# Optimization experiments

Hardware: AMD Instinct MI355X
Metric: run time of the kernel (lower is better)

Reference implementation:

```python
import jax, jax.numpy as jnp
import numpy as np

Q_AA = 21    # amino acids + gap
D_REP = 64   # representation dim
H = 32       # heads
L = 256      # sequence length
DK = 32
DV = 32
M = 8192     # number of MSA sequences
LAMBDA = 1e-3


def setup_inputs() -> dict:
    key = jax.random.key(0)
    ks = jax.random.split(key, 6)
    return {
        "reps_matrix": jax.random.normal(ks[0], (Q_AA, D_REP), jnp.float32),
        "Q": jax.random.normal(ks[1], (H, L, DK), jnp.float32),
        "K": jax.random.normal(ks[2], (H, L, DK), jnp.float32),
        "V_metric": jax.random.normal(ks[3], (H, D_REP, DV), jnp.float32),
        "Z": jax.random.randint(ks[4], (L, M), 0, Q_AA),
        "weights": jax.random.uniform(ks[5], (M,), jnp.float32),
    }


def reference(reps_matrix, Q, K, V_metric, Z, weights):
    dk = Q.shape[-1]
    # symmetrized per-head attention map (no mask)
    scores = jnp.einsum('hid,hjd->hij', Q, K) / jnp.sqrt(jnp.asarray(dk, Q.dtype))
    probs = jax.nn.softmax(scores, axis=-1)
    A = 0.5 * (probs + jnp.swapaxes(probs, -1, -2))        # (H, L, L)

    # V_aa via RBF kernel on V1 = reps_matrix @ V_metric
    V1 = jnp.einsum('qd,hdv->hqv', reps_matrix, V_metric)  # (H, q, dv)
    gamma = 1.0 / V1.shape[1]  # torch code uses 1/X.shape[1] == 1/q
    sq = jnp.sum(V1 * V1, axis=-1)                          # (H, q)
    D2 = sq[:, :, None] + sq[:, None, :] - 2.0 * jnp.einsum('hqv,hav->hqa', V1, V1)
    Vaa = jnp.exp(-gamma * jnp.maximum(D2, 0.0))           # (H, q, q)

    # coupling tensor J with zeroed diagonal (i == j)
    J = jnp.einsum('hij,hqa->ijqa', A, Vaa)                # (L, L, q, q)
    off_diag = 1.0 - jnp.eye(J.shape[0], dtype=J.dtype)
    J = J * off_diag[:, :, None, None]

    q = Vaa.shape[1]
    Zoh = jax.nn.one_hot(Z, q, dtype=J.dtype)              # (L, M, q)
    # energy[state, position, sequence] = sum_{j,a} J[r,j,state,a] * onehot(Z)[j,m,a]
    E = jnp.einsum('rjqa,jma->qrm', J, Zoh)                # (q, L, M)
    lge = jax.nn.logsumexp(E, axis=0)                      # (L, M)
    E_correct = jnp.take_along_axis(E, Z[None], axis=0)[0] # (L, M)

    pl = -jnp.sum(weights * jnp.sum(E_correct - lge, axis=0))
    reg = LAMBDA * jnp.sum(J * J)
    return pl + reg
```

## Files before the change

### kernel.cpp

```cpp
#include <hip/hip_runtime.h>
#include <hip/hip_bf16.h>

#define H_ 32
#define L_ 256
#define DK_ 32
#define DV_ 32
#define QAA 21
#define AQ_ 441
#define DREP 64
#define M_ 8192
#define LAMBDA_ 1e-3f

#define JSTR 56
#define JJSTR 1184
#define JCH 8
#define CHUNK_B (JCH * JJSTR)
#define NCH (L_ / JCH)

#define JC 8
#define TM 4

__global__ __launch_bounds__(256) void softmax_kernel(const float* __restrict__ Q,
                                                      const float* __restrict__ K,
                                                      float* __restrict__ P) {
  const int i = blockIdx.x, h = blockIdx.y, j = threadIdx.x;
  __shared__ float qrow[DK_];
  __shared__ float red[256];
  if (j < DK_) qrow[j] = Q[(h * L_ + i) * DK_ + j];
  __syncthreads();
  const float* krow = &K[(h * L_ + j) * DK_];
  float s = 0.f;
#pragma unroll
  for (int d = 0; d < DK_; ++d) s += qrow[d] * krow[d];
  s *= 0.17677669529663687f;
  red[j] = s;
  __syncthreads();
  for (int t = 128; t > 0; t >>= 1) {
    if (j < t) red[j] = fmaxf(red[j], red[j + t]);
    __syncthreads();
  }
  const float mx = red[0];
  __syncthreads();
  const float e = __expf(s - mx);
  red[j] = e;
  __syncthreads();
  for (int t = 128; t > 0; t >>= 1) {
    if (j < t) red[j] += red[j + t];
    __syncthreads();
  }
  P[(h * L_ + i) * L_ + j] = e / red[0];
}

__global__ __launch_bounds__(256) void sym_kernel(const float* __restrict__ P,
                                                  float* __restrict__ A) {
  const int idx = blockIdx.x * 256 + threadIdx.x;
  const int h = idx >> 16;
  const int i = (idx >> 8) & 255;
  const int j = idx & 255;
  A[idx] = 0.5f * (P[idx] + P[(h << 16) | (j << 8) | i]);
}

__global__ __launch_bounds__(256) void vaa_kernel(const float* __restrict__ reps,
                                                  const float* __restrict__ Vm,
                                                  float* __restrict__ Vaa) {
  const int h = blockIdx.x;
  __shared__ float V1[QAA * DV_];
  __shared__ float sq[QAA];
  for (int e = threadIdx.x; e < QAA * DV_; e += 256) {
    const int q = e >> 5, v = e & 31;
    float acc = 0.f;
#pragma unroll
    for (int d = 0; d < DREP; ++d) acc += reps[q * DREP + d] * Vm[(h * DREP + d) * DV_ + v];
    V1[e] = acc;
  }
  __syncthreads();
  if (threadIdx.x < QAA) {
    float acc = 0.f;
#pragma unroll
    for (int v = 0; v < DV_; ++v) { const float x = V1[threadIdx.x * DV_ + v]; acc += x * x; }
    sq[threadIdx.x] = acc;
  }
  __syncthreads();
  const float gamma = 1.f / 21.f;
  for (int e = threadIdx.x; e < AQ_; e += 256) {
    const int qq = e / QAA, aa = e - qq * QAA;
    float dot = 0.f;
#pragma unroll
    for (int v = 0; v < DV_; ++v) dot += V1[qq * DV_ + v] * V1[aa * DV_ + v];
    const float d2 = sq[qq] + sq[aa] - 2.f * dot;
    Vaa[h * AQ_ + e] = __expf(-gamma * fmaxf(d2, 0.f));
  }
}

__global__ __launch_bounds__(256) void reg_kernel(const float* __restrict__ A,
                                                  const float* __restrict__ Vaa,
                                                  float* __restrict__ out) {
  const int h1 = blockIdx.x >> 5, h2 = blockIdx.x & 31;
  const float* A1 = A + h1 * (L_ * L_);
  const float* A2 = A + h2 * (L_ * L_);
  float s = 0.f;
  for (int idx = threadIdx.x; idx < L_ * L_; idx += 256) s += A1[idx] * A2[idx];
  s -= A1[threadIdx.x * (L_ + 1)] * A2[threadIdx.x * (L_ + 1)];
  float g = 0.f;
  const float* V1 = Vaa + h1 * AQ_;
  const float* V2 = Vaa + h2 * AQ_;
  for (int e = threadIdx.x; e < AQ_; e += 256) g += V1[e] * V2[e];
  __shared__ float redS[256], redG[256];
  redS[threadIdx.x] = s; redG[threadIdx.x] = g;
  __syncthreads();
  for (int t = 128; t > 0; t >>= 1) {
    if (threadIdx.x < t) {
      redS[threadIdx.x] += redS[threadIdx.x + t];
      redG[threadIdx.x] += redG[threadIdx.x + t];
    }
    __syncthreads();
  }
  if (threadIdx.x == 0) atomicAdd(out, LAMBDA_ * redS[0] * redG[0]);
}

static __device__ inline unsigned bf16_bits(float x) {
  __hip_bfloat16 b = __float2bfloat16(x);
  unsigned short u;
  __builtin_memcpy(&u, &b, 2);
  return (unsigned)u;
}

__global__ __launch_bounds__(256) void jbuild_kernel(const float* __restrict__ A,
                                                     const float* __restrict__ Vaa,
                                                     unsigned char* __restrict__ Jg) {
  __shared__ float AT[L_ * H_];
  const int r = blockIdx.x, tid = threadIdx.x;
#pragma unroll
  for (int i = 0; i < H_; ++i) AT[tid * H_ + i] = A[(i * L_ + r) * L_ + tid];

  const int s = tid;
  const bool active = (s < 252);
  int a = 0, w = 0;
  if (active) { a = s / 12; w = s - a * 12; }
  const int q0 = 2 * w, q1 = q0 + 1;
  float vh0[H_], vh1[H_];
#pragma unroll
  for (int h = 0; h < H_; ++h) {
    vh0[h] = (active && q0 < QAA) ? Vaa[h * AQ_ + a * QAA + q0] : 0.f;
    vh1[h] = (active && q1 < QAA) ? Vaa[h * AQ_ + a * QAA + q1] : 0.f;
  }
  __syncthreads();

  unsigned char* dst = Jg + (size_t)r * (L_ * JJSTR);
  const int byte_off = a * JSTR + w * 4;
  for (int j = 0; j < L_; ++j) {
    float v0 = 0.f, v1 = 0.f;
    const float4* Ar4 = (const float4*)&AT[j * H_];
#pragma unroll
    for (int h4 = 0; h4 < H_ / 4; ++h4) {
      const float4 a4 = Ar4[h4];
      v0 += a4.x * vh0[h4 * 4 + 0]; v1 += a4.x * vh1[h4 * 4 + 0];
      v0 += a4.y * vh0[h4 * 4 + 1]; v1 += a4.y * vh1[h4 * 4 + 1];
      v0 += a4.z * vh0[h4 * 4 + 2]; v1 += a4.z * vh1[h4 * 4 + 2];
      v0 += a4.w * vh0[h4 * 4 + 3]; v1 += a4.w * vh1[h4 * 4 + 3];
    }
    if (j == r) { v0 = 0.f; v1 = 0.f; }
    if (active) {
      const unsigned u = bf16_bits(v0) | (bf16_bits(v1) << 16);
      *(unsigned*)(dst + (size_t)(j * JJSTR + byte_off)) = u;
    }
  }
}

__global__ __launch_bounds__(256) void gather_kernel(const unsigned char* __restrict__ Jg,
                                                     const int* __restrict__ Z,
                                                     const float* __restrict__ W,
                                                     float* __restrict__ out) {
  __shared__ __align__(16) unsigned char buf[CHUNK_B];
  __shared__ float red[256];
  const int r = blockIdx.x, tid = threadIdx.x;
  const int mb = blockIdx.y * 1024 + tid * 4;
  const unsigned char* Jr = Jg + (size_t)r * (L_ * JJSTR);

  float E[TM][QAA];
#pragma unroll
  for (int k = 0; k < TM; ++k)
#pragma unroll
    for (int q = 0; q < QAA; ++q) E[k][q] = 0.f;

  uint4 st0, st1, st2;
  const int i0 = tid, i1 = 256 + tid, i2 = 512 + tid;
  const bool v2 = (i2 * 16 < CHUNK_B);
  {
    const unsigned char* src = Jr;
    st0 = *(const uint4*)(src + i0 * 16);
    st1 = *(const uint4*)(src + i1 * 16);
    if (v2) st2 = *(const uint4*)(src + i2 * 16);
  }

  for (int c = 0; c < NCH; ++c) {
    __syncthreads();
    *(uint4*)(buf + i0 * 16) = st0;
    *(uint4*)(buf + i1 * 16) = st1;
    if (v2) *(uint4*)(buf + i2 * 16) = st2;
    __syncthreads();
    if (c + 1 < NCH) {
      const unsigned char* src = Jr + (size_t)(c + 1) * CHUNK_B;
      st0 = *(const uint4*)(src + i0 * 16);
      st1 = *(const uint4*)(src + i1 * 16);
      if (v2) st2 = *(const uint4*)(src + i2 * 16);
    }
    for (int jj = 0; jj < JCH; ++jj) {
      const int j = c * JCH + jj;
      const int4 za = *(const int4*)(Z + j * M_ + mb);
      const int aa[TM] = {za.x, za.y, za.z, za.w};
#pragma unroll
      for (int k = 0; k < TM; ++k) {
        const unsigned char* row = buf + jj * JJSTR + aa[k] * JSTR;
        const uint2 g0 = *(const uint2*)(row + 0);
        const uint2 g1 = *(const uint2*)(row + 8);
        const uint2 g2 = *(const uint2*)(row + 16);
        const uint2 g3 = *(const uint2*)(row + 24);
        const uint2 g4 = *(const uint2*)(row + 32);
        const uint2 g5 = *(const uint2*)(row + 40);
        const unsigned wv[11] = {g0.x, g0.y, g1.x, g1.y, g2.x, g2.y,
                                 g3.x, g3.y, g4.x, g4.y, g5.x};
#pragma unroll
        for (int p = 0; p < 10; ++p) {
          const unsigned u = wv[p];
          const unsigned lo = u << 16, hi = u & 0xFFFF0000u;
          E[k][2 * p]     += __int_as_float((int)lo);
          E[k][2 * p + 1] += __int_as_float((int)hi);
        }
        E[k][20] += __int_as_float((int)(wv[10] << 16));
      }
    }
  }

  const int4 zr = *(const int4*)(Z + r * M_ + mb);
  const int zra[TM] = {zr.x, zr.y, zr.z, zr.w};
  const float4 w4 = *(const float4*)(W + mb);
  const float wa[TM] = {w4.x, w4.y, w4.z, w4.w};
  float contrib = 0.f;
#pragma unroll
  for (int k = 0; k < TM; ++k) {
    float mx = E[k][0];
#pragma unroll
    for (int q = 1; q < QAA; ++q) mx = fmaxf(mx, E[k][q]);
    float s = 0.f;
#pragma unroll
    for (int q = 0; q < QAA; ++q) s += __expf(E[k][q] - mx);
    const float lge = mx + __logf(s);
    float Ec = E[k][0];
#pragma unroll
    for (int q = 1; q < QAA; ++q) Ec = (zra[k] == q) ? E[k][q] : Ec;
    contrib += wa[k] * (Ec - lge);
  }
  red[tid] = contrib;
  __syncthreads();
  for (int t = 128; t > 0; t >>= 1) {
    if (tid < t) red[tid] += red[tid + t];
    __syncthreads();
  }
  if (tid == 0) atomicAdd(out, -red[0]);
}

__global__ __launch_bounds__(256) void main_kernel(const float* __restrict__ A,
                                                   const float* __restrict__ Vaa,
                                                   const int* __restrict__ Z,
                                                   const float* __restrict__ W,
                                                   float* __restrict__ out) {
  __shared__ float A_r[H_ * L_];
  __shared__ float J_s[JC * AQ_];
  __shared__ float red[256];

  const int r = blockIdx.x;
  const int tid = threadIdx.x;
  const int mbase = blockIdx.y * (TM * 256) + tid;

  for (int e = tid; e < H_ * L_; e += 256) {
    const int h = e >> 8, j = e & 255;
    A_r[e] = A[(h * L_ + r) * L_ + j];
  }
  const int aq0 = tid, aq1 = tid + 256;
  const bool has1 = (aq1 < AQ_);
  float vh0[H_], vh1[H_];
#pragma unroll
  for (int h = 0; h < H_; ++h) {
    vh0[h] = Vaa[h * AQ_ + aq0];
    vh1[h] = has1 ? Vaa[h * AQ_ + aq1] : 0.f;
  }
  __syncthreads();

  float E[TM][QAA];
#pragma unroll
  for (int k = 0; k < TM; ++k)
#pragma unroll
    for (int q = 0; q < QAA; ++q) E[k][q] = 0.f;

  for (int j0 = 0; j0 < L_; j0 += JC) {
#pragma unroll
    for (int jj = 0; jj < JC; ++jj) {
      const int j = j0 + jj;
      float v0 = 0.f, v1 = 0.f;
#pragma unroll
      for (int h = 0; h < H_; ++h) {
        const float a = A_r[h * L_ + j];
        v0 += a * vh0[h];
        v1 += a * vh1[h];
      }
      if (j == r) { v0 = 0.f; v1 = 0.f; }
      J_s[jj * AQ_ + aq0] = v0;
      if (has1) J_s[jj * AQ_ + aq1] = v1;
    }
    __syncthreads();
#pragma unroll
    for (int jj = 0; jj < JC; ++jj) {
      const int j = j0 + jj;
      int a[TM];
#pragma unroll
      for (int k = 0; k < TM; ++k) a[k] = Z[j * M_ + mbase + k * 256];
#pragma unroll
      for (int k = 0; k < TM; ++k) {
        const float* row = &J_s[jj * AQ_ + a[k] * QAA];
#pragma unroll
        for (int q = 0; q < QAA; ++q) E[k][q] += row[q];
      }
    }
    __syncthreads();
  }

  float contrib = 0.f;
#pragma unroll
  for (int k = 0; k < TM; ++k) {
    const int m = mbase + k * 256;
    float mx = -1e30f;
#pragma unroll
    for (int q = 0; q < QAA; ++q) mx = fmaxf(mx, E[k][q]);
    float s = 0.f;
#pragma unroll
    for (int q = 0; q < QAA; ++q) s += __expf(E[k][q] - mx);
    const float lge = mx + __logf(s);
    const int zr = Z[r * M_ + m];
    float Ec = 0.f;
#pragma unroll
    for (int q = 0; q < QAA; ++q) Ec = (q == zr) ? E[k][q] : Ec;
    contrib += W[m] * (Ec - lge);
  }
  red[tid] = contrib;
  __syncthreads();
  for (int t = 128; t > 0; t >>= 1) {
    if (tid < t) red[tid] += red[tid + t];
    __syncthreads();
  }
  if (tid == 0) atomicAdd(out, -red[0]);
}

extern "C" void kernel_launch(void* const* d_in, const int* in_sizes, int n_in,
                              void* d_out, int out_size, void* d_ws, size_t ws_size,
                              hipStream_t stream) {
  const float* reps = (const float*)d_in[0];
  const float* Q    = (const float*)d_in[1];
  const float* K    = (const float*)d_in[2];
  const float* Vm   = (const float*)d_in[3];
  const int*   Z    = (const int*)d_in[4];
  const float* W    = (const float*)d_in[5];
  float* out = (float*)d_out;

  float* P   = (float*)d_ws;
  float* A   = P + H_ * L_ * L_;
  float* Vaa = A + H_ * L_ * L_;
  (void)in_sizes; (void)n_in; (void)out_size;

  const size_t base = (size_t)2 * H_ * L_ * L_ * 4 + (size_t)H_ * AQ_ * 4;
  const size_t jg_off = (base + 255) & ~(size_t)255;
  const size_t need = jg_off + (size_t)L_ * L_ * JJSTR;

  hipMemsetAsync(out, 0, sizeof(float), stream);
  softmax_kernel<<<dim3(L_, H_), 256, 0, stream>>>(Q, K, P);
  sym_kernel<<<(H_ * L_ * L_) / 256, 256, 0, stream>>>(P, A);
  vaa_kernel<<<H_, 256, 0, stream>>>(reps, Vm, Vaa);
  reg_kernel<<<H_ * H_, 256, 0, stream>>>(A, Vaa, out);

  if (ws_size >= need) {
    unsigned char* Jg = (unsigned char*)d_ws + jg_off;
    jbuild_kernel<<<L_, 256, 0, stream>>>(A, Vaa, Jg);
    gather_kernel<<<dim3(L_, M_ / 1024), 256, 0, stream>>>(Jg, Z, W, out);
  } else {
    main_kernel<<<dim3(L_, M_ / (TM * 256)), 256, 0, stream>>>(A, Vaa, Z, W, out);
  }
}
```

Before: 954.7 us.

## Double-buffer J chunks via direct global-to-LDS loads, tighten J row stride, tile sym transpose

The gather kernel now double-buffers the J chunk in shared memory using global_load_lds, so the next chunk streams straight into LDS while the current one is consumed. This drops one barrier and the register staging per chunk. The per-amino-acid row stride shrinks from 56 to 52 bytes, which reduces J storage and traffic; jbuild is adjusted to match. Accumulation uses packed float2 vectors, and the symmetrize kernel becomes a shared-memory tiled transpose so its reads are coalesced. In exchange, the doubled LDS buffer and a min-blocks launch bound change occupancy, and the code depends on correct synchronisation of the async LDS loads.

Result: faster. 871.7 us (-8.7%).

```diff
diff --git a/kernel.cpp b/kernel.cpp
--- a/kernel.cpp
+++ b/kernel.cpp
@@ -1,5 +1,8 @@
 #include <hip/hip_runtime.h>
 #include <hip/hip_bf16.h>
+
+typedef unsigned int uint;
+typedef float v2f __attribute__((ext_vector_type(2)));
 
 #define H_ 32
 #define L_ 256
@@ -11,10 +14,11 @@
 #define M_ 8192
 #define LAMBDA_ 1e-3f
 
-#define JSTR 56
-#define JJSTR 1184
+#define JSTR 52
+#define JJSTR 1104
 #define JCH 8
 #define CHUNK_B (JCH * JJSTR)
+#define NGRAN (CHUNK_B / 16)
 #define NCH (L_ / JCH)
 
 #define JC 8
@@ -53,11 +57,22 @@
 
 __global__ __launch_bounds__(256) void sym_kernel(const float* __restrict__ P,
                                                   float* __restrict__ A) {
-  const int idx = blockIdx.x * 256 + threadIdx.x;
-  const int h = idx >> 16;
-  const int i = (idx >> 8) & 255;
-  const int j = idx & 255;
-  A[idx] = 0.5f * (P[idx] + P[(h << 16) | (j << 8) | i]);
+  __shared__ float t1[32][33], t2[32][33];
+  const int h = blockIdx.z;
+  const int i0 = blockIdx.x * 32, j0 = blockIdx.y * 32;
+  const int tx = threadIdx.x, ty = threadIdx.y;
+#pragma unroll
+  for (int ry = 0; ry < 4; ++ry) {
+    const int row = ty + ry * 8;
+    t1[row][tx] = P[(h * L_ + i0 + row) * L_ + j0 + tx];
+    t2[row][tx] = P[(h * L_ + j0 + row) * L_ + i0 + tx];
+  }
+  __syncthreads();
+#pragma unroll
+  for (int ry = 0; ry < 4; ++ry) {
+    const int row = ty + ry * 8;
+    A[(h * L_ + i0 + row) * L_ + j0 + tx] = 0.5f * (t1[row][tx] + t2[tx][row]);
+  }
 }
 
 __global__ __launch_bounds__(256) void vaa_kernel(const float* __restrict__ reps,
@@ -134,9 +149,9 @@
   for (int i = 0; i < H_; ++i) AT[tid * H_ + i] = A[(i * L_ + r) * L_ + tid];
 
   const int s = tid;
-  const bool active = (s < 252);
+  const bool active = (s < 231);
   int a = 0, w = 0;
-  if (active) { a = s / 12; w = s - a * 12; }
+  if (active) { a = s / 11; w = s - a * 11; }
   const int q0 = 2 * w, q1 = q0 + 1;
   float vh0[H_], vh1[H_];
 #pragma unroll
@@ -167,67 +182,60 @@
   }
 }
 
-__global__ __launch_bounds__(256) void gather_kernel(const unsigned char* __restrict__ Jg,
-                                                     const int* __restrict__ Z,
-                                                     const float* __restrict__ W,
-                                                     float* __restrict__ out) {
-  __shared__ __align__(16) unsigned char buf[CHUNK_B];
+#define GLOAD16(ldst, gsrc)                                                            \
+  __builtin_amdgcn_global_load_lds((const __attribute__((address_space(1))) void*)(gsrc), \
+                                   (__attribute__((address_space(3))) void*)(ldst), 16, 0, 0)
+
+__global__ __launch_bounds__(256, 3) void gather_kernel(const unsigned char* __restrict__ Jg,
+                                                        const int* __restrict__ Z,
+                                                        const float* __restrict__ W,
+                                                        float* __restrict__ out) {
+  __shared__ __align__(16) unsigned char buf[2][CHUNK_B];
   __shared__ float red[256];
   const int r = blockIdx.x, tid = threadIdx.x;
   const int mb = blockIdx.y * 1024 + tid * 4;
   const unsigned char* Jr = Jg + (size_t)r * (L_ * JJSTR);
 
-  float E[TM][QAA];
+  v2f E2[TM][11];
 #pragma unroll
   for (int k = 0; k < TM; ++k)
 #pragma unroll
-    for (int q = 0; q < QAA; ++q) E[k][q] = 0.f;
-
-  uint4 st0, st1, st2;
-  const int i0 = tid, i1 = 256 + tid, i2 = 512 + tid;
-  const bool v2 = (i2 * 16 < CHUNK_B);
+    for (int w = 0; w < 11; ++w) E2[k][w] = (v2f){0.f, 0.f};
+
   {
     const unsigned char* src = Jr;
-    st0 = *(const uint4*)(src + i0 * 16);
-    st1 = *(const uint4*)(src + i1 * 16);
-    if (v2) st2 = *(const uint4*)(src + i2 * 16);
+    GLOAD16(&buf[0][tid * 16], src + tid * 16);
+    GLOAD16(&buf[0][(tid + 256) * 16], src + (tid + 256) * 16);
+    if (tid < NGRAN - 512) GLOAD16(&buf[0][(tid + 512) * 16], src + (tid + 512) * 16);
   }
 
   for (int c = 0; c < NCH; ++c) {
-    __syncthreads();
-    *(uint4*)(buf + i0 * 16) = st0;
-    *(uint4*)(buf + i1 * 16) = st1;
-    if (v2) *(uint4*)(buf + i2 * 16) = st2;
     __syncthreads();
     if (c + 1 < NCH) {
       const unsigned char* src = Jr + (size_t)(c + 1) * CHUNK_B;
-      st0 = *(const uint4*)(src + i0 * 16);
-      st1 = *(const uint4*)(src + i1 * 16);
-      if (v2) st2 = *(const uint4*)(src + i2 * 16);
-    }
+      unsigned char* db = buf[(c + 1) & 1];
+      GLOAD16(db + tid * 16, src + tid * 16);
+      GLOAD16(db + (tid + 256) * 16, src + (tid + 256) * 16);
+      if (tid < NGRAN - 512) GLOAD16(db + (tid + 512) * 16, src + (tid + 512) * 16);
+    }
+    const unsigned char* pb = buf[c & 1];
     for (int jj = 0; jj < JCH; ++jj) {
       const int j = c * JCH + jj;
       const int4 za = *(const int4*)(Z + j * M_ + mb);
       const int aa[TM] = {za.x, za.y, za.z, za.w};
 #pragma unroll
       for (int k = 0; k < TM; ++k) {
-        const unsigned char* row = buf + jj * JJSTR + aa[k] * JSTR;
-        const uint2 g0 = *(const uint2*)(row + 0);
-        const uint2 g1 = *(const uint2*)(row + 8);
-        const uint2 g2 = *(const uint2*)(row + 16);
-        const uint2 g3 = *(const uint2*)(row + 24);
-        const uint2 g4 = *(const uint2*)(row + 32);
-        const uint2 g5 = *(const uint2*)(row + 40);
-        const unsigned wv[11] = {g0.x, g0.y, g1.x, g1.y, g2.x, g2.y,
-                                 g3.x, g3.y, g4.x, g4.y, g5.x};
-#pragma unroll
-        for (int p = 0; p < 10; ++p) {
-          const unsigned u = wv[p];
-          const unsigned lo = u << 16, hi = u & 0xFFFF0000u;
-          E[k][2 * p]     += __int_as_float((int)lo);
-          E[k][2 * p + 1] += __int_as_float((int)hi);
+        const uint* row = (const uint*)(pb + jj * JJSTR + aa[k] * JSTR);
+        uint u[11];
+#pragma unroll
+        for (int w = 0; w < 11; ++w) u[w] = row[w];
+#pragma unroll
+        for (int w = 0; w < 11; ++w) {
+          v2f t;
+          t.x = __uint_as_float(u[w] << 16);
+          t.y = __uint_as_float(u[w] & 0xFFFF0000u);
+          E2[k][w] += t;
         }
-        E[k][20] += __int_as_float((int)(wv[10] << 16));
       }
     }
   }
@@ -239,16 +247,20 @@
   float contrib = 0.f;
 #pragma unroll
   for (int k = 0; k < TM; ++k) {
-    float mx = E[k][0];
-#pragma unroll
-    for (int q = 1; q < QAA; ++q) mx = fmaxf(mx, E[k][q]);
+    float ev[QAA];
+#pragma unroll
+    for (int w = 0; w < 10; ++w) { ev[2 * w] = E2[k][w].x; ev[2 * w + 1] = E2[k][w].y; }
+    ev[20] = E2[k][10].x;
+    float mx = ev[0];
+#pragma unroll
+    for (int q = 1; q < QAA; ++q) mx = fmaxf(mx, ev[q]);
     float s = 0.f;
 #pragma unroll
-    for (int q = 0; q < QAA; ++q) s += __expf(E[k][q] - mx);
+    for (int q = 0; q < QAA; ++q) s += __expf(ev[q] - mx);
     const float lge = mx + __logf(s);
-    float Ec = E[k][0];
-#pragma unroll
-    for (int q = 1; q < QAA; ++q) Ec = (zra[k] == q) ? E[k][q] : Ec;
+    float Ec = ev[0];
+#pragma unroll
+    for (int q = 1; q < QAA; ++q) Ec = (zra[k] == q) ? ev[q] : Ec;
     contrib += wa[k] * (Ec - lge);
   }
   red[tid] = contrib;
@@ -373,7 +385,7 @@
 
   hipMemsetAsync(out, 0, sizeof(float), stream);
   softmax_kernel<<<dim3(L_, H_), 256, 0, stream>>>(Q, K, P);
-  sym_kernel<<<(H_ * L_ * L_) / 256, 256, 0, stream>>>(P, A);
+  sym_kernel<<<dim3(8, 8, H_), dim3(32, 8), 0, stream>>>(P, A);
   vaa_kernel<<<H_, 256, 0, stream>>>(reps, Vm, Vaa);
   reg_kernel<<<H_ * H_, 256, 0, stream>>>(A, Vaa, out);
 
```
